# Kernel tuning notes

Measured on AMD Instinct MI355X. Metric: run time of the kernel, lower is better.

## Reference

```python
import jax, jax.numpy as jnp
import numpy as np
from jax import lax

B = 32768
L = 200          # window_size
K = 5            # conv kernel
CIN = 6
FLAT = L - K + 1  # 196, conv1d valid output length (out channels = 1)


def setup_inputs() -> dict:
    key = jax.random.key(0)
    ks = jax.random.split(key, 9)
    s = lambda *sh: 1.0 / np.sqrt(sh[-1])
    x = jax.random.normal(ks[0], (B, CIN, L), dtype=jnp.float32)
    conv_w = jax.random.normal(ks[1], (1, CIN, K), dtype=jnp.float32) * (1.0 / np.sqrt(CIN * K))
    conv_b = jax.random.normal(ks[2], (1,), dtype=jnp.float32) * 0.1
    w1 = jax.random.normal(ks[3], (FLAT, 50), dtype=jnp.float32) * (1.0 / np.sqrt(FLAT))
    b1 = jax.random.normal(ks[4], (50,), dtype=jnp.float32) * 0.1
    w2 = jax.random.normal(ks[5], (50, 30), dtype=jnp.float32) * (1.0 / np.sqrt(50))
    b2 = jax.random.normal(ks[6], (30,), dtype=jnp.float32) * 0.1
    w3 = jax.random.normal(ks[7], (30, 15), dtype=jnp.float32) * (1.0 / np.sqrt(30))
    b3 = jax.random.normal(ks[8], (15,), dtype=jnp.float32) * 0.1
    return {"x": x, "conv_w": conv_w, "conv_b": conv_b, "w1": w1, "b1": b1,
            "w2": w2, "b2": b2, "w3": w3, "b3": b3}


def reference(x, conv_w, conv_b, w1, b1, w2, b2, w3, b3):
    # conv1d (valid): [B,6,200] -> [B,1,196]
    y = lax.conv_general_dilated(x, conv_w, window_strides=(1,), padding='VALID',
                                 dimension_numbers=('NCH', 'OIH', 'NCH'))
    y = y + conv_b[None, :, None]
    h = y.reshape(x.shape[0], -1)                       # [B,196]
    h = jax.nn.relu(h @ w1 + b1)                        # [B,50]
    h = jax.nn.relu(h @ w2 + b2)                        # [B,30]
    out = h @ w3 + b3                                   # [B,15]
    # Procrustes orthogonalization of the 3x3 block
    R = out[:, :9].reshape(-1, 3, 3)
    U, _, VT = jnp.linalg.svd(R)                        # batched 3x3 SVD
    det = jnp.linalg.det(jnp.matmul(U, VT))             # [B]
    scale = jnp.stack([jnp.ones_like(det), jnp.ones_like(det), det], axis=1)  # diag(1,1,det)
    R_norm = jnp.matmul(U, VT * scale[:, :, None])      # U @ S @ VT
    return jnp.concatenate([R_norm.reshape(-1, 9), out[:, 9:]], axis=1)
```

## Files before the change

### kernel.cpp

```cpp
#include <hip/hip_runtime.h>
#include <math.h>

#define BATCH 32768
#define LW    200
#define CIN   6
#define KSZ   5
#define FLAT  196
#define NH1   50
#define NH2   30
#define NOUT  15
#define ROWP  201

__global__ __launch_bounds__(256) void fused_kernel(
    const float* __restrict__ x,
    const float* __restrict__ cw, const float* __restrict__ cb,
    const float* __restrict__ w1, const float* __restrict__ b1,
    const float* __restrict__ w2, const float* __restrict__ b2,
    const float* __restrict__ w3, const float* __restrict__ b3,
    float* __restrict__ out)
{
    __shared__ float xs[64 * ROWP];

    const int tid  = threadIdx.x;
    const int wv   = __builtin_amdgcn_readfirstlane(tid >> 6);
    const int lane = tid & 63;
    const int b    = blockIdx.x * 64 + lane;
    const int kstart = 49 * wv;

    float w[CIN][KSZ];
#pragma unroll
    for (int c = 0; c < CIN; ++c)
#pragma unroll
        for (int k = 0; k < KSZ; ++k) w[c][k] = cw[c * KSZ + k];

    const int bb0 = (tid >= 200) ? 1 : 0;
    const int i0  = tid - 200 * bb0;
    const float* xblk = x + (size_t)blockIdx.x * 64 * (CIN * LW);

    float acc[49];
    const float bias = cb[0];
#pragma unroll
    for (int i = 0; i < 49; ++i) acc[i] = bias;

    for (int ch = 0; ch < CIN; ++ch) {
        __syncthreads();

        {
            int i  = i0;
            int go = bb0 * (CIN * LW) + ch * LW + i0;
            int lo = bb0 * ROWP + i0;
            for (int kb = 0; kb < 5; ++kb) {
                float v[10]; int lof[10];
#pragma unroll
                for (int u = 0; u < 10; ++u) {
                    v[u] = xblk[go];
                    lof[u] = lo;
                    bool two = (i >= 144);
                    i  += two ? -144 : 56;
                    go += two ? 2 * (CIN * LW) - 144 : (CIN * LW) + 56;
                    lo += two ? 2 * ROWP - 144 : ROWP + 56;
                }
#pragma unroll
                for (int u = 0; u < 10; ++u) xs[lof[u]] = v[u];
            }
        }
        __syncthreads();

        const float* row = xs + lane * ROWP + kstart;
        float x0 = row[0], x1 = row[1], x2 = row[2], x3 = row[3];
#pragma unroll
        for (int i = 0; i < 49; ++i) {
            float x4v = row[i + 4];
            float a = acc[i];
            a = fmaf(x0, w[ch][0], a);
            a = fmaf(x1, w[ch][1], a);
            a = fmaf(x2, w[ch][2], a);
            a = fmaf(x3, w[ch][3], a);
            a = fmaf(x4v, w[ch][4], a);
            acc[i] = a;
            x0 = x1; x1 = x2; x2 = x3; x3 = x4v;
        }
    }

    float h1p[NH1];
#pragma unroll
    for (int j = 0; j < NH1; ++j) h1p[j] = 0.f;
#pragma unroll
    for (int ii = 0; ii < 49; ++ii) {
        const float* wrow = w1 + (size_t)(kstart + ii) * NH1;
        float c = acc[ii];
#pragma unroll
        for (int j = 0; j < NH1; ++j) h1p[j] = fmaf(c, wrow[j], h1p[j]);
    }

    __syncthreads();
    float* part = xs;
    if (wv != 0) {
#pragma unroll
        for (int j = 0; j < NH1; ++j)
            part[(size_t)(wv - 1) * (64 * 53) + lane * 53 + j] = h1p[j];
    }
    __syncthreads();
    if (wv != 0) return;

    float h1[NH1];
#pragma unroll
    for (int j = 0; j < NH1; ++j) {
        float s = h1p[j]
                + part[lane * 53 + j]
                + part[64 * 53 + lane * 53 + j]
                + part[2 * 64 * 53 + lane * 53 + j]
                + b1[j];
        h1[j] = fmaxf(s, 0.f);
    }

    float h2[NH2];
#pragma unroll
    for (int j = 0; j < NH2; ++j) h2[j] = b2[j];
#pragma unroll
    for (int k = 0; k < NH1; ++k) {
        float hk = h1[k];
        const float* row = w2 + k * NH2;
#pragma unroll
        for (int j = 0; j < NH2; ++j) h2[j] = fmaf(hk, row[j], h2[j]);
    }
#pragma unroll
    for (int j = 0; j < NH2; ++j) h2[j] = fmaxf(h2[j], 0.f);

    float o[NOUT];
#pragma unroll
    for (int j = 0; j < NOUT; ++j) o[j] = b3[j];
#pragma unroll
    for (int k = 0; k < NH2; ++k) {
        float hk = h2[k];
        const float* row = w3 + k * NOUT;
#pragma unroll
        for (int j = 0; j < NOUT; ++j) o[j] = fmaf(hk, row[j], o[j]);
    }

    {
        float r00 = o[0], r01 = o[1], r02 = o[2];
        float r10 = o[3], r11 = o[4], r12 = o[5];
        float r20 = o[6], r21 = o[7], r22 = o[8];

        float A[4][4], V[4][4];
        A[0][0] = r00 + r11 + r22;
        A[1][1] = r00 - r11 - r22;
        A[2][2] = r11 - r00 - r22;
        A[3][3] = r22 - r00 - r11;
        A[0][1] = A[1][0] = r21 - r12;
        A[0][2] = A[2][0] = r02 - r20;
        A[0][3] = A[3][0] = r10 - r01;
        A[1][2] = A[2][1] = r01 + r10;
        A[1][3] = A[3][1] = r02 + r20;
        A[2][3] = A[3][2] = r12 + r21;
#pragma unroll
        for (int i = 0; i < 4; ++i)
#pragma unroll
            for (int j = 0; j < 4; ++j) V[i][j] = (i == j) ? 1.f : 0.f;

        const int pr[6][2] = {{0,1},{0,2},{0,3},{1,2},{1,3},{2,3}};
        for (int sweep = 0; sweep < 7; ++sweep) {
#pragma unroll
            for (int pi = 0; pi < 6; ++pi) {
                const int p = pr[pi][0], q = pr[pi][1];
                float apq = A[p][q];
                if (fabsf(apq) > 1e-20f) {
                    float theta = (A[q][q] - A[p][p]) / (2.f * apq);
                    float t = copysignf(1.f, theta) / (fabsf(theta) + sqrtf(1.f + theta * theta));
                    float c = rsqrtf(1.f + t * t);
                    float s = t * c;
#pragma unroll
                    for (int k = 0; k < 4; ++k) {
                        float akp = A[k][p], akq = A[k][q];
                        A[k][p] = c * akp - s * akq;
                        A[k][q] = s * akp + c * akq;
                    }
#pragma unroll
                    for (int k = 0; k < 4; ++k) {
                        float apk = A[p][k], aqk = A[q][k];
                        A[p][k] = c * apk - s * aqk;
                        A[q][k] = s * apk + c * aqk;
                    }
#pragma unroll
                    for (int k = 0; k < 4; ++k) {
                        float vkp = V[k][p], vkq = V[k][q];
                        V[k][p] = c * vkp - s * vkq;
                        V[k][q] = s * vkp + c * vkq;
                    }
                }
            }
        }

        int best = 0;
        float bl = A[0][0];
#pragma unroll
        for (int i = 1; i < 4; ++i)
            if (A[i][i] > bl) { bl = A[i][i]; best = i; }

        float vw = V[0][best], vx = V[1][best], vy = V[2][best], vz = V[3][best];
        float inv = rsqrtf(vw * vw + vx * vx + vy * vy + vz * vz);
        vw *= inv; vx *= inv; vy *= inv; vz *= inv;

        float xx = vx * vx, yy = vy * vy, zz = vz * vz;
        float xy = vx * vy, xz = vx * vz, yz = vy * vz;
        float wx = vw * vx, wy = vw * vy, wz = vw * vz;

        float* ob = out + (long)b * NOUT;
        ob[0]  = 1.f - 2.f * (yy + zz);
        ob[1]  = 2.f * (xy - wz);
        ob[2]  = 2.f * (xz + wy);
        ob[3]  = 2.f * (xy + wz);
        ob[4]  = 1.f - 2.f * (xx + zz);
        ob[5]  = 2.f * (yz - wx);
        ob[6]  = 2.f * (xz - wy);
        ob[7]  = 2.f * (yz + wx);
        ob[8]  = 1.f - 2.f * (xx + yy);
        ob[9]  = o[9];
        ob[10] = o[10];
        ob[11] = o[11];
        ob[12] = o[12];
        ob[13] = o[13];
        ob[14] = o[14];
    }
}

extern "C" void kernel_launch(void* const* d_in, const int* in_sizes, int n_in,
                              void* d_out, int out_size, void* d_ws, size_t ws_size,
                              hipStream_t stream) {
    const float* x  = (const float*)d_in[0];
    const float* cw = (const float*)d_in[1];
    const float* cb = (const float*)d_in[2];
    const float* w1 = (const float*)d_in[3];
    const float* b1 = (const float*)d_in[4];
    const float* w2 = (const float*)d_in[5];
    const float* b2 = (const float*)d_in[6];
    const float* w3 = (const float*)d_in[7];
    const float* b3 = (const float*)d_in[8];
    float* outp = (float*)d_out;

    fused_kernel<<<BATCH / 64, 256, 0, stream>>>(x, cw, cb, w1, b1, w2, b2, w3, b3, outp);
}
```

Before: 314.2 us.

## Give each wave a private float4-loaded input tile with register prefetch, dropping barriers

Each of the four waves now stages only the 56-float slice of every row it needs into its own LDS tile, using float4 global loads, instead of the whole block cooperatively staging a full 200-wide row per channel. The next channel's data is prefetched into registers while the current channel is convolved, and the two per-channel __syncthreads are removed. This aims to cut barrier stalls and exposed global-load latency, at the cost of slightly more LDS, some redundant overlapping loads between waves, and relying on in-wave ordering of LDS accesses without an explicit barrier.

```diff
diff --git a/kernel.cpp b/kernel.cpp
--- a/kernel.cpp
+++ b/kernel.cpp
@@ -9,7 +9,8 @@
 #define NH1   50
 #define NH2   30
 #define NOUT  15
-#define ROWP  201
+#define TILEW 57
+#define NLD   14
 
 __global__ __launch_bounds__(256) void fused_kernel(
     const float* __restrict__ x,
@@ -19,54 +20,59 @@
     const float* __restrict__ w3, const float* __restrict__ b3,
     float* __restrict__ out)
 {
-    __shared__ float xs[64 * ROWP];
+    __shared__ float xs[4 * 64 * TILEW];
 
     const int tid  = threadIdx.x;
     const int wv   = __builtin_amdgcn_readfirstlane(tid >> 6);
     const int lane = tid & 63;
     const int b    = blockIdx.x * 64 + lane;
     const int kstart = 49 * wv;
+    const int tbase  = 48 * wv;
+    const int off    = wv;
+
+    float* tile = xs + wv * (64 * TILEW);
 
     float w[CIN][KSZ];
 #pragma unroll
     for (int c = 0; c < CIN; ++c)
 #pragma unroll
         for (int k = 0; k < KSZ; ++k) w[c][k] = cw[c * KSZ + k];
-
-    const int bb0 = (tid >= 200) ? 1 : 0;
-    const int i0  = tid - 200 * bb0;
-    const float* xblk = x + (size_t)blockIdx.x * 64 * (CIN * LW);
+    const float bias = cb[0];
+
+    int goff[NLD];
+    int loff[NLD];
+#pragma unroll
+    for (int u = 0; u < NLD; ++u) {
+        int g   = lane + 64 * u;
+        int row = g / NLD;
+        int c4  = g - row * NLD;
+        goff[u] = row * (CIN * LW) + 4 * c4;
+        loff[u] = row * TILEW + 4 * c4;
+    }
+    const float* xw = x + (size_t)blockIdx.x * 64 * (CIN * LW) + tbase;
 
     float acc[49];
-    const float bias = cb[0];
 #pragma unroll
     for (int i = 0; i < 49; ++i) acc[i] = bias;
 
+    float4 buf[NLD];
+#pragma unroll
+    for (int u = 0; u < NLD; ++u)
+        buf[u] = *(const float4*)(xw + goff[u]);
+
+#pragma unroll
     for (int ch = 0; ch < CIN; ++ch) {
-        __syncthreads();
-
-        {
-            int i  = i0;
-            int go = bb0 * (CIN * LW) + ch * LW + i0;
-            int lo = bb0 * ROWP + i0;
-            for (int kb = 0; kb < 5; ++kb) {
-                float v[10]; int lof[10];
-#pragma unroll
-                for (int u = 0; u < 10; ++u) {
-                    v[u] = xblk[go];
-                    lof[u] = lo;
-                    bool two = (i >= 144);
-                    i  += two ? -144 : 56;
-                    go += two ? 2 * (CIN * LW) - 144 : (CIN * LW) + 56;
-                    lo += two ? 2 * ROWP - 144 : ROWP + 56;
-                }
-#pragma unroll
-                for (int u = 0; u < 10; ++u) xs[lof[u]] = v[u];
-            }
-        }
-        __syncthreads();
-
-        const float* row = xs + lane * ROWP + kstart;
+#pragma unroll
+        for (int u = 0; u < NLD; ++u) {
+            float* dst = tile + loff[u];
+            dst[0] = buf[u].x; dst[1] = buf[u].y; dst[2] = buf[u].z; dst[3] = buf[u].w;
+        }
+        if (ch + 1 < CIN) {
+#pragma unroll
+            for (int u = 0; u < NLD; ++u)
+                buf[u] = *(const float4*)(xw + (ch + 1) * LW + goff[u]);
+        }
+        const float* row = tile + lane * TILEW + off;
         float x0 = row[0], x1 = row[1], x2 = row[2], x3 = row[3];
 #pragma unroll
         for (int i = 0; i < 49; ++i) {
@@ -98,7 +104,7 @@
     if (wv != 0) {
 #pragma unroll
         for (int j = 0; j < NH1; ++j)
-            part[(size_t)(wv - 1) * (64 * 53) + lane * 53 + j] = h1p[j];
+            part[(wv - 1) * (64 * 53) + lane * 53 + j] = h1p[j];
     }
     __syncthreads();
     if (wv != 0) return;
```

New measurement: 298.2 us. 1.05x faster.
